# Performance work log

Measured on AMD Instinct MI355X. Metric: run time of the kernel, lower is better.

Reference implementation:

```python
import jax, jax.numpy as jnp
import numpy as np


def _make_pert(r, s):
    lin = np.linspace(-r, r, s)
    xm, ym, tm = np.meshgrid(lin, lin, lin)  # default 'xy' indexing, matches torch code
    return jnp.asarray(np.stack([xm.ravel(), ym.ravel(), tm.ravel()], axis=-1), dtype=jnp.float32)

PERTS = (_make_pert(0.01, 3), _make_pert(0.05, 5), _make_pert(0.09, 7))  # [27,3],[125,3],[343,3]

N, IN, H, HQ, FF, OUT = 4096, 3, 256, 64, 64, 3


def setup_inputs():
    key = jax.random.key(0)
    ks = jax.random.split(key, 24)

    def W(k, i, o):
        return (jax.random.normal(k, (i, o), jnp.float32) / np.sqrt(i)).astype(jnp.float32)

    one = jnp.ones((1,), jnp.float32)
    return {
        "x": jax.random.normal(ks[0], (N, 1), jnp.float32),
        "y": jax.random.normal(ks[1], (N, 1), jnp.float32),
        "t": jax.random.normal(ks[2], (N, 1), jnp.float32),
        # linear_emb: 3 -> 64 -> WaveAct -> 256
        "emb_W1": W(ks[3], IN, HQ), "emb_b1": jnp.zeros((HQ,), jnp.float32),
        "emb_wa": one, "emb_wb": one,
        "emb_W2": W(ks[4], HQ, H), "emb_b2": jnp.zeros((H,), jnp.float32),
        # multiregion_mixer: 4 -> 8 -> WaveAct -> 1
        "mix_W1": W(ks[5], 4, 8), "mix_b1": jnp.zeros((8,), jnp.float32),
        "mix_wa": one, "mix_wb": one,
        "mix_W2": W(ks[6], 8, 1), "mix_b2": jnp.zeros((1,), jnp.float32),
        "out_W0": W(ks[7], H, FF), "out_b0": jnp.zeros((FF,), jnp.float32),
        "out_wa0": one, "out_wb0": one,
        "out_Wh": jnp.stack([W(ks[8 + i], FF, FF) for i in range(3)]),
        "out_bh": jnp.zeros((3, FF), jnp.float32),
        "out_wah": jnp.ones((3, 1), jnp.float32), "out_wbh": jnp.ones((3, 1), jnp.float32),
        "out_Wf1": W(ks[11], FF, FF), "out_bf1": jnp.zeros((FF,), jnp.float32),
        "out_waf": one, "out_wbf": one,
        "out_Wf2": W(ks[12], FF, OUT), "out_bf2": jnp.zeros((OUT,), jnp.float32),
    }


def _wave(h, wa, wb):
    return wa * jnp.sin(h) + wb * jnp.cos(h)


def reference(x, y, t,
              emb_W1, emb_b1, emb_wa, emb_wb, emb_W2, emb_b2,
              mix_W1, mix_b1, mix_wa, mix_wb, mix_W2, mix_b2,
              out_W0, out_b0, out_wa0, out_wb0,
              out_Wh, out_bh, out_wah, out_wbh,
              out_Wf1, out_bf1, out_waf, out_wbf, out_Wf2, out_bf2):
    def emb(s):  # [..., 3] -> [..., 256]
        h = _wave(s @ emb_W1 + emb_b1, emb_wa, emb_wb)
        return h @ emb_W2 + emb_b2

    src = jnp.concatenate([x, y, t], axis=-1)           # [N, 3]
    feats = [emb(src)]                                   # region 1: unperturbed
    for P in PERTS:
        perturbed = src[:, None, :] + P[None, :, :]      # [N, P, 3]
        feats.append(emb(perturbed).mean(axis=1))        # [N, 256]
    stacked = jnp.stack(feats, axis=-1)                  # [N, 256, 4] (== permute(0,2,1) of stack dim=1)

    m = _wave(stacked @ mix_W1 + mix_b1, mix_wa, mix_wb) # [N, 256, 8]
    e = (m @ mix_W2 + mix_b2)[:, :, 0]                   # [N, 256]

    h = _wave(e @ out_W0 + out_b0, out_wa0, out_wb0)     # [N, 64]
    for i in range(3):                                   # fixed num_layer-1 = 3 hidden layers
        h = _wave(h @ out_Wh[i] + out_bh[i], out_wah[i], out_wbh[i])
    h = _wave(h @ out_Wf1 + out_bf1, out_waf, out_wbf)
    return h @ out_Wf2 + out_bf2                         # [N, 3]
```

## Files before the change

kernel.cpp:

```cpp
#include <hip/hip_runtime.h>

#define SPB 2

__global__ __launch_bounds__(256, 8) void model_fused(
    const float* __restrict__ x, const float* __restrict__ y, const float* __restrict__ t,
    const float* __restrict__ embW1, const float* __restrict__ embb1,
    const float* __restrict__ embwa, const float* __restrict__ embwb,
    const float* __restrict__ embW2, const float* __restrict__ embb2,
    const float* __restrict__ mixW1, const float* __restrict__ mixb1,
    const float* __restrict__ mixwa, const float* __restrict__ mixwb,
    const float* __restrict__ mixW2, const float* __restrict__ mixb2,
    const float* __restrict__ outW0, const float* __restrict__ outb0,
    const float* __restrict__ outwa0, const float* __restrict__ outwb0,
    const float* __restrict__ outWh, const float* __restrict__ outbh,
    const float* __restrict__ outwah, const float* __restrict__ outwbh,
    const float* __restrict__ outWf1, const float* __restrict__ outbf1,
    const float* __restrict__ outwaf, const float* __restrict__ outwbf,
    const float* __restrict__ outWf2, const float* __restrict__ outbf2,
    float* __restrict__ out, int N)
{
    __shared__ float sC[3][64];
    __shared__ float sw[SPB][64];
    __shared__ float se[SPB][256];
    __shared__ float pf[2][SPB][64];
    __shared__ float sh[2][SPB][64];
    __shared__ float sMixW1[32], sMixb1[8], sMixW2[8];

    const int tid = threadIdx.x;
    const int n0  = blockIdx.x * SPB;

    if (tid < 32)       sMixW1[tid]      = mixW1[tid];
    else if (tid < 40)  sMixb1[tid - 32] = mixb1[tid - 32];
    else if (tid < 48)  sMixW2[tid - 40] = mixW2[tid - 40];

    {
        const int ch = tid & 63;
        const int sm = tid >> 6;
        const float w0 = embW1[ch], w1 = embW1[64 + ch], w2 = embW1[128 + ch];
        if (sm < SPB) {
            const int n  = n0 + sm;
            const int ns = (n < N) ? n : (N - 1);
            float u = x[ns]*w0 + y[ns]*w1 + t[ns]*w2 + embb1[ch];
            sw[sm][ch] = embwa[0]*__sinf(u) + embwb[0]*__cosf(u);
        } else if (sm == 2) {
            float ga = (1.f + 2.f*__cosf(0.01f*w0))
                     * (1.f + 2.f*__cosf(0.01f*w1))
                     * (1.f + 2.f*__cosf(0.01f*w2)) * (1.f/27.f);
            float gb = (1.f + 2.f*(__cosf(0.025f*w0) + __cosf(0.05f*w0)))
                     * (1.f + 2.f*(__cosf(0.025f*w1) + __cosf(0.05f*w1)))
                     * (1.f + 2.f*(__cosf(0.025f*w2) + __cosf(0.05f*w2))) * (1.f/125.f);
            sC[0][ch] = ga; sC[1][ch] = gb;
        } else {
            float gc = (1.f + 2.f*(__cosf(0.03f*w0) + __cosf(0.06f*w0) + __cosf(0.09f*w0)))
                     * (1.f + 2.f*(__cosf(0.03f*w1) + __cosf(0.06f*w1) + __cosf(0.09f*w1)))
                     * (1.f + 2.f*(__cosf(0.03f*w2) + __cosf(0.06f*w2) + __cosf(0.09f*w2))) * (1.f/343.f);
            sC[2][ch] = gc;
        }
    }
    __syncthreads();

    {
        const int c = tid;
        float a00=0.f,a01=0.f,a02=0.f,a03=0.f;
        float a10=0.f,a11=0.f,a12=0.f,a13=0.f;

        #pragma unroll 8
        for (int ch = 0; ch < 64; ++ch) {
            const float wr = embW2[ch*256 + c];
            const float c1 = sC[0][ch], c2 = sC[1][ch], c3 = sC[2][ch];
            const float t0 = sw[0][ch] * wr;
            const float t1 = sw[1][ch] * wr;
            a00 += t0; a01 = fmaf(t0, c1, a01); a02 = fmaf(t0, c2, a02); a03 = fmaf(t0, c3, a03);
            a10 += t1; a11 = fmaf(t1, c1, a11); a12 = fmaf(t1, c2, a12); a13 = fmaf(t1, c3, a13);
        }

        const float mwa = mixwa[0], mwb = mixwb[0], mb2 = mixb2[0];
        const float bb2 = embb2[c];
        {
            const float s0 = a00+bb2, s1 = a01+bb2, s2 = a02+bb2, s3 = a03+bb2;
            float ev = mb2;
            #pragma unroll
            for (int j = 0; j < 8; ++j) {
                float p = fmaf(s0, sMixW1[j],
                          fmaf(s1, sMixW1[8 + j],
                          fmaf(s2, sMixW1[16 + j],
                          fmaf(s3, sMixW1[24 + j], sMixb1[j]))));
                ev = fmaf(mwa*__sinf(p) + mwb*__cosf(p), sMixW2[j], ev);
            }
            se[0][c] = ev;
        }
        {
            const float s0 = a10+bb2, s1 = a11+bb2, s2 = a12+bb2, s3 = a13+bb2;
            float ev = mb2;
            #pragma unroll
            for (int j = 0; j < 8; ++j) {
                float p = fmaf(s0, sMixW1[j],
                          fmaf(s1, sMixW1[8 + j],
                          fmaf(s2, sMixW1[16 + j],
                          fmaf(s3, sMixW1[24 + j], sMixb1[j]))));
                ev = fmaf(mwa*__sinf(p) + mwb*__cosf(p), sMixW2[j], ev);
            }
            se[1][c] = ev;
        }
    }
    __syncthreads();

    {
        const int h = tid >> 7;
        const int r = tid & 127;
        const int n = r >> 6, f = r & 63;
        const int k0 = h * 128;
        float p = 0.f;
        #pragma unroll 8
        for (int k = 0; k < 128; ++k)
            p = fmaf(se[n][k0 + k], outW0[(k0 + k)*64 + f], p);
        pf[h][n][f] = p;
    }
    __syncthreads();

    const int n = (tid >> 6) & 1, f = tid & 63;
    if (tid < 128) {
        float a = pf[0][n][f] + pf[1][n][f] + outb0[f];
        sh[0][n][f] = outwa0[0]*__sinf(a) + outwb0[0]*__cosf(a);
    }
    __syncthreads();

    int cur = 0;
    #pragma unroll
    for (int i = 0; i < 3; ++i) {
        if (tid < 128) {
            float a = outbh[i*64 + f];
            const float* W = outWh + i*4096;
            #pragma unroll 8
            for (int k = 0; k < 64; ++k)
                a = fmaf(sh[cur][n][k], W[k*64 + f], a);
            sh[1 - cur][n][f] = outwah[i]*__sinf(a) + outwbh[i]*__cosf(a);
        }
        __syncthreads();
        cur ^= 1;
    }
    if (tid < 128) {
        float a = outbf1[f];
        #pragma unroll 8
        for (int k = 0; k < 64; ++k)
            a = fmaf(sh[cur][n][k], outWf1[k*64 + f], a);
        sh[1 - cur][n][f] = outwaf[0]*__sinf(a) + outwbf[0]*__cosf(a);
    }
    __syncthreads();
    cur ^= 1;

    if (tid < SPB*3) {
        const int nn = tid / 3, o = tid - nn*3;
        float a = outbf2[o];
        #pragma unroll 8
        for (int k = 0; k < 64; ++k)
            a = fmaf(sh[cur][nn][k], outWf2[k*3 + o], a);
        const int gn = n0 + nn;
        if (gn < N) out[gn*3 + o] = a;
    }
}

extern "C" void kernel_launch(void* const* d_in, const int* in_sizes, int n_in,
                              void* d_out, int out_size, void* d_ws, size_t ws_size,
                              hipStream_t stream) {
    const float* x      = (const float*)d_in[0];
    const float* y      = (const float*)d_in[1];
    const float* t      = (const float*)d_in[2];
    const float* embW1  = (const float*)d_in[3];
    const float* embb1  = (const float*)d_in[4];
    const float* embwa  = (const float*)d_in[5];
    const float* embwb  = (const float*)d_in[6];
    const float* embW2  = (const float*)d_in[7];
    const float* embb2  = (const float*)d_in[8];
    const float* mixW1  = (const float*)d_in[9];
    const float* mixb1  = (const float*)d_in[10];
    const float* mixwa  = (const float*)d_in[11];
    const float* mixwb  = (const float*)d_in[12];
    const float* mixW2  = (const float*)d_in[13];
    const float* mixb2  = (const float*)d_in[14];
    const float* outW0  = (const float*)d_in[15];
    const float* outb0  = (const float*)d_in[16];
    const float* outwa0 = (const float*)d_in[17];
    const float* outwb0 = (const float*)d_in[18];
    const float* outWh  = (const float*)d_in[19];
    const float* outbh  = (const float*)d_in[20];
    const float* outwah = (const float*)d_in[21];
    const float* outwbh = (const float*)d_in[22];
    const float* outWf1 = (const float*)d_in[23];
    const float* outbf1 = (const float*)d_in[24];
    const float* outwaf = (const float*)d_in[25];
    const float* outwbf = (const float*)d_in[26];
    const float* outWf2 = (const float*)d_in[27];
    const float* outbf2 = (const float*)d_in[28];
    float* out = (float*)d_out;

    const int N = in_sizes[0];
    const int blocks = (N + SPB - 1) / SPB;
    model_fused<<<blocks, 256, 0, stream>>>(
        x, y, t,
        embW1, embb1, embwa, embwb, embW2, embb2,
        mixW1, mixb1, mixwa, mixwb, mixW2, mixb2,
        outW0, outb0, outwa0, outwb0,
        outWh, outbh, outwah, outwbh,
        outWf1, outbf1, outwaf, outwbf, outWf2, outbf2,
        out, N);
}
```

Measured before the change: 146.8 us.

## Precompute bf16-packed MLP weights and perturbation factors; use readlane broadcasts and split-K layers

Adds a preprocess kernel that packs the output-MLP weights into bf16 pairs and precomputes the per-channel perturbation averaging factors into workspace. The main kernel then uses wavefront readlane broadcasts instead of shared memory for the embedding activations, and splits every 64-wide hidden layer across all 256 threads with a two-way K split. Weights are read at half the bytes, and the first-phase shared stores and barrier are gone. In exchange it adds a second launch, reduces weight precision to bf16, and adds an extra barrier per hidden layer.

```diff
diff --git a/kernel.cpp b/kernel.cpp
--- a/kernel.cpp
+++ b/kernel.cpp
@@ -1,6 +1,64 @@
 #include <hip/hip_runtime.h>
 
 #define SPB 2
+
+__device__ __forceinline__ float rl(float v, int l) {
+    return __builtin_bit_cast(float, __builtin_amdgcn_readlane(__builtin_bit_cast(int, v), l));
+}
+__device__ __forceinline__ float blo(unsigned d) { return __builtin_bit_cast(float, d << 16); }
+__device__ __forceinline__ float bhi(unsigned d) { return __builtin_bit_cast(float, d & 0xffff0000u); }
+__device__ __forceinline__ unsigned pack_bf16(float a, float b) {
+    unsigned ua = __builtin_bit_cast(unsigned, a);
+    unsigned ub = __builtin_bit_cast(unsigned, b);
+    ua = (ua + 0x7fffu + ((ua >> 16) & 1u)) >> 16;
+    ub = (ub + 0x7fffu + ((ub >> 16) & 1u)) >> 16;
+    return ua | (ub << 16);
+}
+
+#define WS_C    0
+#define WS_W0P  256
+#define WS_WHP  (256 + 8192)
+#define WS_WF1P (256 + 8192 + 6144)
+
+__global__ __launch_bounds__(256) void preprocess(
+    const float* __restrict__ embW1,
+    const float* __restrict__ outW0, const float* __restrict__ outWh,
+    const float* __restrict__ outWf1, unsigned* __restrict__ ws)
+{
+    const int g = blockIdx.x * 256 + threadIdx.x;
+    if (g < 8192) {
+        const int k2 = g >> 6, f = g & 63;
+        ws[WS_W0P + g] = pack_bf16(outW0[(2*k2)*64 + f], outW0[(2*k2+1)*64 + f]);
+    } else if (g < 14336) {
+        const int i = g - 8192;
+        const int layer = i >> 11, r = i & 2047;
+        const int k2 = r >> 6, f = r & 63;
+        const float* W = outWh + layer*4096;
+        ws[WS_WHP + i] = pack_bf16(W[(2*k2)*64 + f], W[(2*k2+1)*64 + f]);
+    } else if (g < 16384) {
+        const int i = g - 14336;
+        const int k2 = i >> 6, f = i & 63;
+        ws[WS_WF1P + i] = pack_bf16(outWf1[(2*k2)*64 + f], outWf1[(2*k2+1)*64 + f]);
+    } else if (g < 16576) {
+        const int i = g - 16384;
+        const int r = i >> 6, ch = i & 63;
+        const float w0 = embW1[ch], w1 = embW1[64 + ch], w2 = embW1[128 + ch];
+        float v;
+        if (r == 0) {
+            v = (1.f + 2.f*__cosf(0.01f*w0)) * (1.f + 2.f*__cosf(0.01f*w1))
+              * (1.f + 2.f*__cosf(0.01f*w2)) * (1.f/27.f);
+        } else if (r == 1) {
+            v = (1.f + 2.f*(__cosf(0.025f*w0) + __cosf(0.05f*w0)))
+              * (1.f + 2.f*(__cosf(0.025f*w1) + __cosf(0.05f*w1)))
+              * (1.f + 2.f*(__cosf(0.025f*w2) + __cosf(0.05f*w2))) * (1.f/125.f);
+        } else {
+            v = (1.f + 2.f*(__cosf(0.03f*w0) + __cosf(0.06f*w0) + __cosf(0.09f*w0)))
+              * (1.f + 2.f*(__cosf(0.03f*w1) + __cosf(0.06f*w1) + __cosf(0.09f*w1)))
+              * (1.f + 2.f*(__cosf(0.03f*w2) + __cosf(0.06f*w2) + __cosf(0.09f*w2))) * (1.f/343.f);
+        }
+        ((float*)ws)[WS_C + i] = v;
+    }
+}
 
 __global__ __launch_bounds__(256, 8) void model_fused(
     const float* __restrict__ x, const float* __restrict__ y, const float* __restrict__ t,
@@ -10,68 +68,52 @@
     const float* __restrict__ mixW1, const float* __restrict__ mixb1,
     const float* __restrict__ mixwa, const float* __restrict__ mixwb,
     const float* __restrict__ mixW2, const float* __restrict__ mixb2,
-    const float* __restrict__ outW0, const float* __restrict__ outb0,
+    const float* __restrict__ outb0,
     const float* __restrict__ outwa0, const float* __restrict__ outwb0,
-    const float* __restrict__ outWh, const float* __restrict__ outbh,
+    const float* __restrict__ outbh,
     const float* __restrict__ outwah, const float* __restrict__ outwbh,
-    const float* __restrict__ outWf1, const float* __restrict__ outbf1,
+    const float* __restrict__ outbf1,
     const float* __restrict__ outwaf, const float* __restrict__ outwbf,
     const float* __restrict__ outWf2, const float* __restrict__ outbf2,
+    const unsigned* __restrict__ ws,
     float* __restrict__ out, int N)
 {
-    __shared__ float sC[3][64];
-    __shared__ float sw[SPB][64];
     __shared__ float se[SPB][256];
     __shared__ float pf[2][SPB][64];
     __shared__ float sh[2][SPB][64];
-    __shared__ float sMixW1[32], sMixb1[8], sMixW2[8];
-
-    const int tid = threadIdx.x;
-    const int n0  = blockIdx.x * SPB;
-
-    if (tid < 32)       sMixW1[tid]      = mixW1[tid];
-    else if (tid < 40)  sMixb1[tid - 32] = mixb1[tid - 32];
-    else if (tid < 48)  sMixW2[tid - 40] = mixW2[tid - 40];
-
+
+    const int tid  = threadIdx.x;
+    const int lane = tid & 63;
+    const int n0   = blockIdx.x * SPB;
+
+    float swv0, swv1, cv1, cv2, cv3;
     {
-        const int ch = tid & 63;
-        const int sm = tid >> 6;
-        const float w0 = embW1[ch], w1 = embW1[64 + ch], w2 = embW1[128 + ch];
-        if (sm < SPB) {
-            const int n  = n0 + sm;
-            const int ns = (n < N) ? n : (N - 1);
-            float u = x[ns]*w0 + y[ns]*w1 + t[ns]*w2 + embb1[ch];
-            sw[sm][ch] = embwa[0]*__sinf(u) + embwb[0]*__cosf(u);
-        } else if (sm == 2) {
-            float ga = (1.f + 2.f*__cosf(0.01f*w0))
-                     * (1.f + 2.f*__cosf(0.01f*w1))
-                     * (1.f + 2.f*__cosf(0.01f*w2)) * (1.f/27.f);
-            float gb = (1.f + 2.f*(__cosf(0.025f*w0) + __cosf(0.05f*w0)))
-                     * (1.f + 2.f*(__cosf(0.025f*w1) + __cosf(0.05f*w1)))
-                     * (1.f + 2.f*(__cosf(0.025f*w2) + __cosf(0.05f*w2))) * (1.f/125.f);
-            sC[0][ch] = ga; sC[1][ch] = gb;
-        } else {
-            float gc = (1.f + 2.f*(__cosf(0.03f*w0) + __cosf(0.06f*w0) + __cosf(0.09f*w0)))
-                     * (1.f + 2.f*(__cosf(0.03f*w1) + __cosf(0.06f*w1) + __cosf(0.09f*w1)))
-                     * (1.f + 2.f*(__cosf(0.03f*w2) + __cosf(0.06f*w2) + __cosf(0.09f*w2))) * (1.f/343.f);
-            sC[2][ch] = gc;
-        }
-    }
-    __syncthreads();
+        const float w0 = embW1[lane], w1 = embW1[64 + lane], w2 = embW1[128 + lane];
+        const float bb = embb1[lane];
+        const float ewa = embwa[0], ewb = embwb[0];
+        const int ns0 = n0;
+        const int ns1 = (n0 + 1 < N) ? n0 + 1 : N - 1;
+        const float u0 = fmaf(x[ns0], w0, fmaf(y[ns0], w1, fmaf(t[ns0], w2, bb)));
+        const float u1 = fmaf(x[ns1], w0, fmaf(y[ns1], w1, fmaf(t[ns1], w2, bb)));
+        swv0 = ewa*__sinf(u0) + ewb*__cosf(u0);
+        swv1 = ewa*__sinf(u1) + ewb*__cosf(u1);
+        const float* C = (const float*)ws + WS_C;
+        cv1 = C[lane]; cv2 = C[64 + lane]; cv3 = C[128 + lane];
+    }
 
     {
         const int c = tid;
         float a00=0.f,a01=0.f,a02=0.f,a03=0.f;
         float a10=0.f,a11=0.f,a12=0.f,a13=0.f;
 
-        #pragma unroll 8
+        #pragma unroll 16
         for (int ch = 0; ch < 64; ++ch) {
-            const float wr = embW2[ch*256 + c];
-            const float c1 = sC[0][ch], c2 = sC[1][ch], c3 = sC[2][ch];
-            const float t0 = sw[0][ch] * wr;
-            const float t1 = sw[1][ch] * wr;
-            a00 += t0; a01 = fmaf(t0, c1, a01); a02 = fmaf(t0, c2, a02); a03 = fmaf(t0, c3, a03);
-            a10 += t1; a11 = fmaf(t1, c1, a11); a12 = fmaf(t1, c2, a12); a13 = fmaf(t1, c3, a13);
+            const float w  = embW2[ch*256 + c];
+            const float s0 = rl(swv0, ch), s1 = rl(swv1, ch);
+            const float k1 = rl(cv1, ch), k2 = rl(cv2, ch), k3 = rl(cv3, ch);
+            const float t0 = s0 * w, t1 = s1 * w;
+            a00 += t0; a01 = fmaf(t0,k1,a01); a02 = fmaf(t0,k2,a02); a03 = fmaf(t0,k3,a03);
+            a10 += t1; a11 = fmaf(t1,k1,a11); a12 = fmaf(t1,k2,a12); a13 = fmaf(t1,k3,a13);
         }
 
         const float mwa = mixwa[0], mwb = mixwb[0], mb2 = mixb2[0];
@@ -81,11 +123,11 @@
             float ev = mb2;
             #pragma unroll
             for (int j = 0; j < 8; ++j) {
-                float p = fmaf(s0, sMixW1[j],
-                          fmaf(s1, sMixW1[8 + j],
-                          fmaf(s2, sMixW1[16 + j],
-                          fmaf(s3, sMixW1[24 + j], sMixb1[j]))));
-                ev = fmaf(mwa*__sinf(p) + mwb*__cosf(p), sMixW2[j], ev);
+                float p = fmaf(s0, mixW1[j],
+                          fmaf(s1, mixW1[8 + j],
+                          fmaf(s2, mixW1[16 + j],
+                          fmaf(s3, mixW1[24 + j], mixb1[j]))));
+                ev = fmaf(mwa*__sinf(p) + mwb*__cosf(p), mixW2[j], ev);
             }
             se[0][c] = ev;
         }
@@ -94,60 +136,65 @@
             float ev = mb2;
             #pragma unroll
             for (int j = 0; j < 8; ++j) {
-                float p = fmaf(s0, sMixW1[j],
-                          fmaf(s1, sMixW1[8 + j],
-                          fmaf(s2, sMixW1[16 + j],
-                          fmaf(s3, sMixW1[24 + j], sMixb1[j]))));
-                ev = fmaf(mwa*__sinf(p) + mwb*__cosf(p), sMixW2[j], ev);
+                float p = fmaf(s0, mixW1[j],
+                          fmaf(s1, mixW1[8 + j],
+                          fmaf(s2, mixW1[16 + j],
+                          fmaf(s3, mixW1[24 + j], mixb1[j]))));
+                ev = fmaf(mwa*__sinf(p) + mwb*__cosf(p), mixW2[j], ev);
             }
             se[1][c] = ev;
         }
     }
     __syncthreads();
 
+    const int h = tid >> 7, n = (tid >> 6) & 1, f = tid & 63;
+
     {
-        const int h = tid >> 7;
-        const int r = tid & 127;
-        const int n = r >> 6, f = r & 63;
-        const int k0 = h * 128;
+        const unsigned* W0p = ws + WS_W0P;
         float p = 0.f;
         #pragma unroll 8
-        for (int k = 0; k < 128; ++k)
-            p = fmaf(se[n][k0 + k], outW0[(k0 + k)*64 + f], p);
+        for (int j = h*32; j < h*32 + 32; ++j) {
+            const float4 a4 = *(const float4*)&se[n][4*j];
+            const unsigned d0 = W0p[(2*j)*64 + f];
+            const unsigned d1 = W0p[(2*j+1)*64 + f];
+            p = fmaf(a4.x, blo(d0), p); p = fmaf(a4.y, bhi(d0), p);
+            p = fmaf(a4.z, blo(d1), p); p = fmaf(a4.w, bhi(d1), p);
+        }
         pf[h][n][f] = p;
     }
     __syncthreads();
-
-    const int n = (tid >> 6) & 1, f = tid & 63;
     if (tid < 128) {
-        float a = pf[0][n][f] + pf[1][n][f] + outb0[f];
+        const float a = pf[0][n][f] + pf[1][n][f] + outb0[f];
         sh[0][n][f] = outwa0[0]*__sinf(a) + outwb0[0]*__cosf(a);
     }
     __syncthreads();
 
     int cur = 0;
     #pragma unroll
-    for (int i = 0; i < 3; ++i) {
+    for (int i = 0; i < 4; ++i) {
+        const unsigned* Wp = (i < 3) ? (ws + WS_WHP + i*2048) : (ws + WS_WF1P);
+        float p = 0.f;
+        #pragma unroll
+        for (int j = 0; j < 8; ++j) {
+            const int jj = h*8 + j;
+            const float4 a4 = *(const float4*)&sh[cur][n][4*jj];
+            const unsigned d0 = Wp[(2*jj)*64 + f];
+            const unsigned d1 = Wp[(2*jj+1)*64 + f];
+            p = fmaf(a4.x, blo(d0), p); p = fmaf(a4.y, bhi(d0), p);
+            p = fmaf(a4.z, blo(d1), p); p = fmaf(a4.w, bhi(d1), p);
+        }
+        pf[h][n][f] = p;
+        __syncthreads();
         if (tid < 128) {
-            float a = outbh[i*64 + f];
-            const float* W = outWh + i*4096;
-            #pragma unroll 8
-            for (int k = 0; k < 64; ++k)
-                a = fmaf(sh[cur][n][k], W[k*64 + f], a);
-            sh[1 - cur][n][f] = outwah[i]*__sinf(a) + outwbh[i]*__cosf(a);
+            float a = pf[0][n][f] + pf[1][n][f];
+            float wa, wb;
+            if (i < 3) { a += outbh[i*64 + f]; wa = outwah[i]; wb = outwbh[i]; }
+            else       { a += outbf1[f];       wa = outwaf[0]; wb = outwbf[0]; }
+            sh[1 - cur][n][f] = wa*__sinf(a) + wb*__cosf(a);
         }
         __syncthreads();
         cur ^= 1;
     }
-    if (tid < 128) {
-        float a = outbf1[f];
-        #pragma unroll 8
-        for (int k = 0; k < 64; ++k)
-            a = fmaf(sh[cur][n][k], outWf1[k*64 + f], a);
-        sh[1 - cur][n][f] = outwaf[0]*__sinf(a) + outwbf[0]*__cosf(a);
-    }
-    __syncthreads();
-    cur ^= 1;
 
     if (tid < SPB*3) {
         const int nn = tid / 3, o = tid - nn*3;
@@ -193,15 +240,19 @@
     const float* outWf2 = (const float*)d_in[27];
     const float* outbf2 = (const float*)d_in[28];
     float* out = (float*)d_out;
+    unsigned* ws = (unsigned*)d_ws;
 
     const int N = in_sizes[0];
+
+    preprocess<<<65, 256, 0, stream>>>(embW1, outW0, outWh, outWf1, ws);
+
     const int blocks = (N + SPB - 1) / SPB;
     model_fused<<<blocks, 256, 0, stream>>>(
         x, y, t,
         embW1, embb1, embwa, embwb, embW2, embb2,
         mixW1, mixb1, mixwa, mixwb, mixW2, mixb2,
-        outW0, outb0, outwa0, outwb0,
-        outWh, outbh, outwah, outwbh,
-        outWf1, outbf1, outwaf, outwbf, outWf2, outbf2,
-        out, N);
-}
+        outb0, outwa0, outwb0,
+        outbh, outwah, outwbh,
+        outbf1, outwaf, outwbf, outWf2, outbf2,
+        ws, out, N);
+}
```

After: 150.1 us. 2.2% more time.
